# Kernel optimization log

Measured on AMD Instinct MI355X. Metric: run time of the kernel, lower is better.

The kernel has to match this reference:

```python
import jax, jax.numpy as jnp
import numpy as np
from jax.scipy.special import xlogy

N = 8_388_608   # B*L flattened tokens
NCATS = 3       # genotype classes 0/1/2
GROUP = 4       # minimac r2 group size
IGNORE = -100


def setup_inputs() -> dict:
    key = jax.random.key(0)
    k1, k2 = jax.random.split(key)
    logits = jax.random.normal(k1, (N, NCATS), dtype=jnp.float32)
    targets = jax.random.randint(k2, (N,), 0, NCATS, dtype=jnp.int32)
    return {"logits": logits, "targets": targets}


def reference(logits, targets):
    log_probs = jax.nn.log_softmax(logits, axis=-1)          # (N, C)
    probs = jnp.exp(log_probs)                               # (N, C)

    valid = targets != IGNORE                                # (N,)
    tgt = jnp.where(valid, targets, 0)

    # CrossEntropyLoss(ignore_index, reduction='sum')
    picked = jnp.take_along_axis(log_probs, tgt[:, None], axis=-1)[:, 0]
    ce_loss = -jnp.sum(jnp.where(valid, picked, 0.0))

    # KLDivLoss(reduction='sum')(log_probs, probs) = sum probs*(log(probs) - log_probs)
    kl_loss = jnp.sum(xlogy(probs, probs) - probs * log_probs)

    # minimac R2 over groups of GROUP consecutive *valid* rows (L == 1).
    alt_p = 1.0 - probs[:, 0]                                # (N,)
    af = tgt.astype(jnp.float32) / 2.0
    edge = (af == 0.0) | (af == 1.0)                         # mask in _r2
    af2 = jnp.where(edge, 0.5, af)
    denom = jnp.maximum(af2 * (1.0 - af2), 0.01)
    sq = (alt_p - af2) ** 2

    w = valid.astype(jnp.float32)
    rank = jnp.cumsum(valid.astype(jnp.int32)) - valid.astype(jnp.int32)
    gid = rank // GROUP                                       # group id among valid rows
    num_groups = N // GROUP + 1

    cnt = jax.ops.segment_sum(w, gid, num_segments=num_groups)         # group sizes
    ssq = jax.ops.segment_sum(sq * w, gid, num_segments=num_groups)
    mse = ssq / jnp.maximum(cnt, 1.0)                                  # per-group mean

    # per-element: where(edge, 0, mse_g/denom); group contribution scaled by cnt_g
    term = w * jnp.where(edge, 0.0, mse[gid] / denom) * cnt[gid]
    r2_loss = -jnp.sum(term)

    return ce_loss + kl_loss + r2_loss
```

## Files before the change

### kernel.cpp

```cpp
#include <hip/hip_runtime.h>


constexpr int IGNORE_IDX = -100;

#define NBLOCKS1 2048
#define THREADS1 256

__global__ __launch_bounds__(THREADS1) void imp_loss_stage1(
    const float* __restrict__ logits,
    const int*   __restrict__ targets,
    float*       __restrict__ partials,
    int ngroups)
{
    const int tid    = blockIdx.x * blockDim.x + threadIdx.x;
    const int stride = gridDim.x * blockDim.x;

    float local = 0.0f;

    for (int gid = tid; gid < ngroups; gid += stride) {
        const float4* lg = reinterpret_cast<const float4*>(logits) + (size_t)gid * 3;
        float4 a = lg[0];
        float4 b = lg[1];
        float4 c = lg[2];
        int4 t4 = reinterpret_cast<const int4*>(targets)[gid];

        float L[4][3] = {
            {a.x, a.y, a.z},
            {a.w, b.x, b.y},
            {b.z, b.w, c.x},
            {c.y, c.z, c.w},
        };
        int T[4] = {t4.x, t4.y, t4.z, t4.w};

        float ce  = 0.0f;
        float ssq = 0.0f;
        float n1  = 0.0f;

        #pragma unroll
        for (int j = 0; j < 4; ++j) {
            float l0 = L[j][0], l1 = L[j][1], l2 = L[j][2];
            float m  = fmaxf(l0, fmaxf(l1, l2));
            float e0 = __expf(l0 - m);
            float e1 = __expf(l1 - m);
            float e2 = __expf(l2 - m);
            float s  = e0 + e1 + e2;
            float lse = m + __logf(s);

            int  t = T[j];
            bool v = (t != IGNORE_IDX);
            float lt = (t == 1) ? l1 : ((t == 2) ? l2 : l0);
            if (v) {
                ce += lse - lt;
                float p0 = e0 * __builtin_amdgcn_rcpf(s);
                float d  = 0.5f - p0;
                ssq += d * d;
                if (t == 1) n1 += 1.0f;
            }
        }
        local += ce - 4.0f * ssq * n1;
    }

    #pragma unroll
    for (int off = 32; off > 0; off >>= 1)
        local += __shfl_down(local, off, 64);

    __shared__ float wsum[THREADS1 / 64];
    const int lane = threadIdx.x & 63;
    const int wid  = threadIdx.x >> 6;
    if (lane == 0) wsum[wid] = local;
    __syncthreads();
    if (threadIdx.x == 0) {
        float s = 0.0f;
        #pragma unroll
        for (int w = 0; w < THREADS1 / 64; ++w) s += wsum[w];
        partials[blockIdx.x] = s;
    }
}

__global__ __launch_bounds__(256) void imp_loss_stage2(
    const float* __restrict__ partials,
    float*       __restrict__ out,
    int n)
{
    float local = 0.0f;
    for (int i = threadIdx.x; i < n; i += 256)
        local += partials[i];

    #pragma unroll
    for (int off = 32; off > 0; off >>= 1)
        local += __shfl_down(local, off, 64);

    __shared__ float wsum[4];
    const int lane = threadIdx.x & 63;
    const int wid  = threadIdx.x >> 6;
    if (lane == 0) wsum[wid] = local;
    __syncthreads();
    if (threadIdx.x == 0)
        out[0] = wsum[0] + wsum[1] + wsum[2] + wsum[3];
}

extern "C" void kernel_launch(void* const* d_in, const int* in_sizes, int n_in,
                              void* d_out, int out_size, void* d_ws, size_t ws_size,
                              hipStream_t stream) {
    const float* logits  = (const float*)d_in[0];
    const int*   targets = (const int*)d_in[1];
    float* out      = (float*)d_out;
    float* partials = (float*)d_ws;

    const int N = in_sizes[1];
    const int ngroups = N / 4;

    imp_loss_stage1<<<NBLOCKS1, THREADS1, 0, stream>>>(logits, targets, partials, ngroups);
    imp_loss_stage2<<<1, 256, 0, stream>>>(partials, out, NBLOCKS1);
}
```

Before: 173.9 us.

## Stage logits through LDS for coalesced loads with register prefetch

```diff
diff --git a/kernel.cpp b/kernel.cpp
--- a/kernel.cpp
+++ b/kernel.cpp
@@ -6,65 +6,115 @@
 #define NBLOCKS1 2048
 #define THREADS1 256
 
+__device__ __forceinline__ float group_term(const float4& a, const float4& b,
+                                            const float4& c, const int4& t4) {
+    float L[4][3] = {
+        {a.x, a.y, a.z},
+        {a.w, b.x, b.y},
+        {b.z, b.w, c.x},
+        {c.y, c.z, c.w},
+    };
+    int T[4] = {t4.x, t4.y, t4.z, t4.w};
+
+    float ce  = 0.0f;
+    float ssq = 0.0f;
+    float n1  = 0.0f;
+
+    #pragma unroll
+    for (int j = 0; j < 4; ++j) {
+        float l0 = L[j][0], l1 = L[j][1], l2 = L[j][2];
+        float m  = fmaxf(l0, fmaxf(l1, l2));
+        float e0 = __expf(l0 - m);
+        float e1 = __expf(l1 - m);
+        float e2 = __expf(l2 - m);
+        float s  = e0 + e1 + e2;
+        float lse = m + __logf(s);
+
+        int  t = T[j];
+        bool v = (t != IGNORE_IDX);
+        float lt = (t == 1) ? l1 : ((t == 2) ? l2 : l0);
+        if (v) {
+            ce += lse - lt;
+            float p0 = e0 * __builtin_amdgcn_rcpf(s);
+            float d  = 0.5f - p0;
+            ssq += d * d;
+            if (t == 1) n1 += 1.0f;
+        }
+    }
+    return ce - 4.0f * ssq * n1;
+}
+
 __global__ __launch_bounds__(THREADS1) void imp_loss_stage1(
     const float* __restrict__ logits,
     const int*   __restrict__ targets,
     float*       __restrict__ partials,
     int ngroups)
 {
-    const int tid    = blockIdx.x * blockDim.x + threadIdx.x;
-    const int stride = gridDim.x * blockDim.x;
+    constexpr int T = THREADS1;
+    constexpr int STRIDE = T + 1;
+    __shared__ float4 lds[3 * STRIDE];
+
+    const int t = threadIdx.x;
+    const float4* __restrict__ lg4 = reinterpret_cast<const float4*>(logits);
+    const int4*   __restrict__ tg4 = reinterpret_cast<const int4*>(targets);
+
+    const int tile = NBLOCKS1 * T;
+    const int full = ngroups / tile;
 
     float local = 0.0f;
 
-    for (int gid = tid; gid < ngroups; gid += stride) {
-        const float4* lg = reinterpret_cast<const float4*>(logits) + (size_t)gid * 3;
-        float4 a = lg[0];
-        float4 b = lg[1];
-        float4 c = lg[2];
-        int4 t4 = reinterpret_cast<const int4*>(targets)[gid];
+    int gbase = blockIdx.x * T;
 
-        float L[4][3] = {
-            {a.x, a.y, a.z},
-            {a.w, b.x, b.y},
-            {b.z, b.w, c.x},
-            {c.y, c.z, c.w},
-        };
-        int T[4] = {t4.x, t4.y, t4.z, t4.w};
+    float4 ca, cb, cc; int4 ct;
+    {
+        size_t f4b = (size_t)gbase * 3;
+        ca = lg4[f4b + t];
+        cb = lg4[f4b + T + t];
+        cc = lg4[f4b + 2 * T + t];
+        ct = tg4[gbase + t];
+    }
 
-        float ce  = 0.0f;
-        float ssq = 0.0f;
-        float n1  = 0.0f;
+    for (int it = 0; it < full; ++it) {
+        float4 na = ca, nb = cb, nc = cc; int4 nt = ct;
+        const int gnext = gbase + tile;
+        if (it + 1 < full) {
+            size_t f4b = (size_t)gnext * 3;
+            na = lg4[f4b + t];
+            nb = lg4[f4b + T + t];
+            nc = lg4[f4b + 2 * T + t];
+            nt = tg4[gnext + t];
+        }
 
-        #pragma unroll
-        for (int j = 0; j < 4; ++j) {
-            float l0 = L[j][0], l1 = L[j][1], l2 = L[j][2];
-            float m  = fmaxf(l0, fmaxf(l1, l2));
-            float e0 = __expf(l0 - m);
-            float e1 = __expf(l1 - m);
-            float e2 = __expf(l2 - m);
-            float s  = e0 + e1 + e2;
-            float lse = m + __logf(s);
+        {
+            const int s0 = t, s1 = t + T, s2 = t + 2 * T;
+            lds[(s0 % 3) * STRIDE + s0 / 3] = ca;
+            lds[(s1 % 3) * STRIDE + s1 / 3] = cb;
+            lds[(s2 % 3) * STRIDE + s2 / 3] = cc;
+        }
+        __syncthreads();
 
-            int  t = T[j];
-            bool v = (t != IGNORE_IDX);
-            float lt = (t == 1) ? l1 : ((t == 2) ? l2 : l0);
-            if (v) {
-                ce += lse - lt;
-                float p0 = e0 * __builtin_amdgcn_rcpf(s);
-                float d  = 0.5f - p0;
-                ssq += d * d;
-                if (t == 1) n1 += 1.0f;
-            }
-        }
-        local += ce - 4.0f * ssq * n1;
+        float4 a = lds[t];
+        float4 b = lds[STRIDE + t];
+        float4 c = lds[2 * STRIDE + t];
+        local += group_term(a, b, c, ct);
+        __syncthreads();
+
+        ca = na; cb = nb; cc = nc; ct = nt;
+        gbase = gnext;
+    }
+
+    for (int g = full * tile + blockIdx.x * T + t; g < ngroups; g += tile) {
+        const float4* lg = lg4 + (size_t)g * 3;
+        float4 a = lg[0], b = lg[1], c = lg[2];
+        int4 t4 = tg4[g];
+        local += group_term(a, b, c, t4);
     }
 
     #pragma unroll
     for (int off = 32; off > 0; off >>= 1)
         local += __shfl_down(local, off, 64);
 
-    __shared__ float wsum[THREADS1 / 64];
+    __shared__ float wsum[T / 64];
     const int lane = threadIdx.x & 63;
     const int wid  = threadIdx.x >> 6;
     if (lane == 0) wsum[wid] = local;
@@ -72,7 +122,7 @@
     if (threadIdx.x == 0) {
         float s = 0.0f;
         #pragma unroll
-        for (int w = 0; w < THREADS1 / 64; ++w) s += wsum[w];
+        for (int w = 0; w < T / 64; ++w) s += wsum[w];
         partials[blockIdx.x] = s;
     }
 }
```

Result: no change. 172.2 us (-1.0%).
